# Optimization experiments

Hardware: AMD Instinct MI355X
Metric: run time of the kernel (lower is better)

The kernel has to match this reference:

```python
import jax, jax.numpy as jnp
import numpy as np

EPS_COS = 1e-8   # torch cosine_similarity eps
ATT_EPS = 1e-6   # LinearAttention eps
LN_EPS = 1e-5    # nn.LayerNorm default eps
NHEAD = 8
WS = 8           # window_size
TOPK = 16
C = 256          # embed_dim (hardcoded 256 in original gather)


def layer_norm(x, w, b):
    m = x.mean(-1, keepdims=True)
    v = ((x - m) ** 2).mean(-1, keepdims=True)
    return (x - m) / jnp.sqrt(v + LN_EPS) * w + b


def linear_attention(q, k, v):
    # q,k,v: [N, L, H, D]
    Q = jax.nn.elu(q) + 1.0
    K = jax.nn.elu(k) + 1.0
    L = v.shape[1]
    v = v / L
    KV = jnp.einsum('nshd,nshv->nhdv', K, v)
    Z = 1.0 / (jnp.einsum('nlhd,nhd->nlh', Q, K.sum(axis=1)) + ATT_EPS)
    return jnp.einsum('nlhd,nhdv,nlh->nlhv', Q, KV, Z) * L


def encoder_layer(x, source, Wq, Wk, Wv, Wm, W1, W2, n1w, n1b, n2w, n2b):
    bs, _, d = x.shape
    dim = d // NHEAD
    q = (x @ Wq).reshape(bs, -1, NHEAD, dim)
    k = (source @ Wk).reshape(bs, -1, NHEAD, dim)
    v = (source @ Wv).reshape(bs, -1, NHEAD, dim)
    msg = linear_attention(q, k, v).reshape(bs, -1, d) @ Wm
    msg = layer_norm(msg, n1w, n1b)
    msg = jax.nn.relu(jnp.concatenate([x, msg], axis=-1) @ W1) @ W2
    msg = layer_norm(msg, n2w, n2b)
    return x + msg


def topk_select(x, k):
    # x: [BN, S, C]; cosine similarity of each token to window mean, then topk
    avg = x.mean(axis=1, keepdims=True)                        # [BN,1,C]
    dot = (avg * x).sum(axis=-1)                               # [BN,S]
    na = jnp.maximum(jnp.linalg.norm(avg, axis=-1), EPS_COS)   # [BN,1]
    nb = jnp.maximum(jnp.linalg.norm(x, axis=-1), EPS_COS)     # [BN,S]
    cos = dot / (na * nb)
    _, idx = jax.lax.top_k(cos, k)                             # [BN,k]
    sel = jnp.take_along_axis(x, idx[:, :, None], axis=1)      # [BN,k,C]
    return sel, idx


def scatter_add(x, idx, src):
    # x: [BN,S,C], idx: [BN,k], src: [BN,k,C]
    BN, S, c = x.shape
    flat_idx = (jnp.arange(BN)[:, None] * S + idx).reshape(-1)
    return x.reshape(BN * S, c).at[flat_idx].add(src.reshape(-1, c)).reshape(BN, S, c)


def window_reverse_nchw(windows, ws, H, W):
    c = windows.shape[-1]
    x = windows.transpose(0, 2, 1).reshape(-1, H // ws, W // ws, c, ws, ws)
    return x.transpose(0, 3, 1, 4, 2, 5).reshape(-1, c, H, W)


def setup_inputs() -> dict:
    key = jax.random.key(0)
    ks = jax.random.split(key, 8)
    BN = 2 * 2304  # batch * nums_window
    s = 1.0 / np.sqrt(C)
    return {
        'x_win_attn': jax.random.normal(ks[0], (BN, WS * WS, C), jnp.float32),
        's_win_attn': jax.random.normal(ks[1], (BN, WS * WS, C), jnp.float32),
        'Wq': jax.random.normal(ks[2], (C, C), jnp.float32) * s,
        'Wk': jax.random.normal(ks[3], (C, C), jnp.float32) * s,
        'Wv': jax.random.normal(ks[4], (C, C), jnp.float32) * s,
        'Wmerge': jax.random.normal(ks[5], (C, C), jnp.float32) * s,
        'W1': jax.random.normal(ks[6], (2 * C, 2 * C), jnp.float32) * (1.0 / np.sqrt(2 * C)),
        'W2': jax.random.normal(ks[7], (2 * C, C), jnp.float32) * (1.0 / np.sqrt(2 * C)),
        'n1w': jnp.ones((C,), jnp.float32),
        'n1b': jnp.zeros((C,), jnp.float32),
        'n2w': jnp.ones((C,), jnp.float32),
        'n2b': jnp.zeros((C,), jnp.float32),
        'batch_size': 2,
        'nums_window': 2304,
        'h': 384,
        'w': 384,
    }


def reference(x_win_attn, s_win_attn, Wq, Wk, Wv, Wmerge, W1, W2,
              n1w, n1b, n2w, n2b, batch_size, nums_window, h, w):
    # 'cross' attention path of WinTopKAttention
    sel1, idx1 = topk_select(x_win_attn, TOPK)
    sel2, _ = topk_select(s_win_attn, TOPK)
    sel1 = sel1.reshape(batch_size, nums_window * TOPK, C)
    sel2 = sel2.reshape(batch_size, nums_window * TOPK, C)
    out = encoder_layer(sel1, sel2, Wq, Wk, Wv, Wmerge, W1, W2, n1w, n1b, n2w, n2b)
    out = out.reshape(batch_size * nums_window, TOPK, C)
    combined = scatter_add(x_win_attn, idx1, out)
    return window_reverse_nchw(combined, WS, h, w)
```

## Files before the change

### kernel.cpp

```cpp
#include <hip/hip_runtime.h>
#include <math.h>

static constexpr int BATCH = 2;
static constexpr int NWIN  = 2304;
static constexpr int BN    = BATCH * NWIN;
static constexpr int S     = 64;
static constexpr int CDIM  = 256;
static constexpr int TOPK_ = 16;
static constexpr int TROWS = BN * TOPK_;
static constexpr int LB    = NWIN * TOPK_;
static constexpr int HW    = 384;
static constexpr int KVSZ  = 8448;
static constexpr int KVB   = 384;
static constexpr int KVTOK = LB / KVB;

typedef unsigned short u16;
typedef __attribute__((ext_vector_type(4))) float  f32x4;
typedef __attribute__((ext_vector_type(8))) short  bf16x8;

__device__ inline u16 f2bf(float f) {
    unsigned u = __float_as_uint(f);
    return (u16)((u + 0x7fffu + ((u >> 16) & 1u)) >> 16);
}
__device__ inline float bf2f(u16 b) {
    return __uint_as_float(((unsigned)b) << 16);
}

__device__ inline void load_lds16(const void* g, void* l) {
    __builtin_amdgcn_global_load_lds(
        (const __attribute__((address_space(1))) unsigned int*)g,
        (__attribute__((address_space(3))) unsigned int*)l, 16, 0, 0);
}

__global__ __launch_bounds__(256) void wconv_all_k(
    const float* __restrict__ Wq, const float* __restrict__ Wk,
    const float* __restrict__ Wv, const float* __restrict__ Wm,
    const float* __restrict__ W1, const float* __restrict__ W2,
    u16* __restrict__ Wqt, u16* __restrict__ Wkt, u16* __restrict__ Wvt,
    u16* __restrict__ Wmt, u16* __restrict__ W1t, u16* __restrict__ W2t)
{
    int t = blockIdx.x * 256 + threadIdx.x;
    const float* W; u16* Wt; int Nd, Kd;
    if (t < 262144) {
        const int sel = t >> 16; t &= 65535;
        W  = (sel == 0 ? Wq  : sel == 1 ? Wk  : sel == 2 ? Wv  : Wm);
        Wt = (sel == 0 ? Wqt : sel == 1 ? Wkt : sel == 2 ? Wvt : Wmt);
        Nd = 256; Kd = 256;
    } else if (t < 524288) { W = W1; Wt = W1t; Nd = 512; Kd = 512; t -= 262144; }
    else                   { W = W2; Wt = W2t; Nd = 256; Kd = 512; t -= 524288; }
    const int k = t / Nd, n = t - k * Nd;
    Wt[(size_t)n * Kd + k] = f2bf(W[t]);
}

__global__ __launch_bounds__(512) void topk_gather_k(
    const float* __restrict__ xin, const float* __restrict__ sin,
    u16* __restrict__ catp, u16* __restrict__ selS, int* __restrict__ idxX)
{
    __shared__ float  win[64 * 256];
    __shared__ double red[2][256];
    __shared__ double avgd[256];
    __shared__ double cosv[64];
    __shared__ int    slots[16];

    const int w    = blockIdx.x;
    const bool isX = (blockIdx.y == 0);
    const int tid  = threadIdx.x;
    const float* src = (isX ? xin : sin) + (size_t)w * S * CDIM;

#pragma unroll
    for (int k = 0; k < 8; ++k) {
        load_lds16(src + k * 2048 + tid * 4,
                   &win[k * 2048 + (tid >> 6) * 256]);
    }
    __syncthreads();

    {
        const int h = tid >> 8, c = tid & 255;
        double sm = 0.0;
        for (int t = h * 32; t < h * 32 + 32; ++t)
            sm += (double)win[t * 256 + c];
        red[h][c] = sm;
    }
    __syncthreads();
    if (tid < 256) avgd[tid] = (red[0][tid] + red[1][tid]) * (1.0 / 64.0);
    __syncthreads();

    {
        const int tok = tid >> 3, p = tid & 7;
        double sd = 0.0, sn = 0.0;
#pragma unroll
        for (int i = 0; i < 8; ++i) {
            const int ic = (i + tok) & 7;
            const int c0 = p * 32 + ic * 4;
            const f32x4 xv4 = *(const f32x4*)&win[tok * 256 + c0];
#pragma unroll
            for (int q = 0; q < 4; ++q) {
                const double xv = (double)xv4[q];
                sd += avgd[c0 + q] * xv;
                sn += xv * xv;
            }
        }
        sd += __shfl_xor(sd, 1); sd += __shfl_xor(sd, 2); sd += __shfl_xor(sd, 4);
        sn += __shfl_xor(sn, 1); sn += __shfl_xor(sn, 2); sn += __shfl_xor(sn, 4);
        if (p == 0) {
            double nb = sqrt(sn); if (nb < 1e-8) nb = 1e-8;
            cosv[tok] = sd / nb;
        }
    }
    __syncthreads();

    if (tid < 64) {
        const double ct = cosv[tid];
        int r = 0;
        for (int j = 0; j < 64; ++j) {
            const double cj = cosv[j];
            r += (cj > ct) || (cj == ct && j < tid);
        }
        if (r < TOPK_) slots[r] = tid;
    }
    __syncthreads();

    const int c = tid & 255, g = tid >> 8;
    if (isX) {
        if (tid < TOPK_) idxX[w * TOPK_ + tid] = slots[tid];
#pragma unroll
        for (int jj = 0; jj < 8; ++jj) {
            const int j = g * 8 + jj;
            catp[((size_t)w * TOPK_ + j) * 512 + c] = f2bf(win[slots[j] * 256 + c]);
        }
    } else {
#pragma unroll
        for (int jj = 0; jj < 8; ++jj) {
            const int j = g * 8 + jj;
            selS[((size_t)w * TOPK_ + j) * 256 + c] = f2bf(win[slots[j] * 256 + c]);
        }
    }
}

template<int EPI>
__device__ inline void gemm_body(
    const u16* __restrict__ A, int lda,
    const u16* __restrict__ Bt, int K,
    u16* __restrict__ Cout, int ldc,
    int m0, int n0, u16* As, u16* Bs)
{
    const int tid = threadIdx.x;
    const int lane = tid & 63, w = tid >> 6;
    const int wr = w >> 1, wc = w & 1;

    f32x4 acc[4][4];
#pragma unroll
    for (int i = 0; i < 4; ++i)
#pragma unroll
        for (int j = 0; j < 4; ++j)
            acc[i][j] = (f32x4){0.f, 0.f, 0.f, 0.f};

    const int rsel = lane & 15, ksel = (lane >> 4) * 8;

    for (int k0 = 0; k0 < K; k0 += 32) {
#pragma unroll
        for (int i = 0; i < 2; ++i) {
            const int c = w * 2 + i;
            const int e = c * 512 + lane * 8;
            const int row = e >> 5, col = e & 31;
            load_lds16(&A[(size_t)(m0 + row) * lda + k0 + col], &As[c * 512]);
            load_lds16(&Bt[(size_t)(n0 + row) * K  + k0 + col], &Bs[c * 512]);
        }
        __syncthreads();

        bf16x8 af[4], bfr[4];
#pragma unroll
        for (int i = 0; i < 4; ++i)
            af[i] = *(const bf16x8*)&As[(wr * 64 + i * 16 + rsel) * 32 + ksel];
#pragma unroll
        for (int j = 0; j < 4; ++j)
            bfr[j] = *(const bf16x8*)&Bs[(wc * 64 + j * 16 + rsel) * 32 + ksel];
#pragma unroll
        for (int i = 0; i < 4; ++i)
#pragma unroll
            for (int j = 0; j < 4; ++j)
                acc[i][j] = __builtin_amdgcn_mfma_f32_16x16x32_bf16(
                    af[i], bfr[j], acc[i][j], 0, 0, 0);
        __syncthreads();
    }

    const int crow = (lane >> 4) * 4, ccol = lane & 15;
#pragma unroll
    for (int i = 0; i < 4; ++i)
#pragma unroll
        for (int j = 0; j < 4; ++j)
#pragma unroll
            for (int r = 0; r < 4; ++r) {
                float v = acc[i][j][r];
                if (EPI == 1) v = (v > 0.f) ? (v + 1.f) : __expf(v);
                if (EPI == 2) v = (v > 0.f) ? v : 0.f;
                Cout[(size_t)(m0 + wr * 64 + i * 16 + crow + r) * ldc
                     + (n0 + wc * 64 + j * 16 + ccol)] = f2bf(v);
            }
}

template<int EPI>
__global__ __launch_bounds__(256) void gemm_bf16_k(
    const u16* __restrict__ A, int lda,
    const u16* __restrict__ Bt, int K,
    u16* __restrict__ Cout, int ldc)
{
    __shared__ u16 As[128 * 32];
    __shared__ u16 Bs[128 * 32];
    gemm_body<EPI>(A, lda, Bt, K, Cout, ldc,
                   blockIdx.y * 128, blockIdx.x * 128, As, Bs);
}

__global__ __launch_bounds__(256) void gemm_qkv_k(
    const u16* __restrict__ catA, const u16* __restrict__ selS,
    const u16* __restrict__ Wqt, const u16* __restrict__ Wkt,
    const u16* __restrict__ Wvt,
    u16* __restrict__ Qb, u16* __restrict__ Kb, u16* __restrict__ Vb)
{
    __shared__ u16 As[128 * 32];
    __shared__ u16 Bs[128 * 32];
    const int z = blockIdx.z;
    if (z == 0)
        gemm_body<1>(catA, 512, Wqt, 256, Qb, 256,
                     blockIdx.y * 128, blockIdx.x * 128, As, Bs);
    else if (z == 1)
        gemm_body<1>(selS, 256, Wkt, 256, Kb, 256,
                     blockIdx.y * 128, blockIdx.x * 128, As, Bs);
    else
        gemm_body<0>(selS, 256, Wvt, 256, Vb, 256,
                     blockIdx.y * 128, blockIdx.x * 128, As, Bs);
}

__global__ __launch_bounds__(256) void kv_part_k(
    const u16* __restrict__ Kb, const u16* __restrict__ Vb,
    float* __restrict__ part)
{
    __shared__ float Kt[16][256];
    __shared__ float Vt[16][256];

    const int bk = blockIdx.x;
    const int batch = bk / KVB, slot = bk % KVB;
    const size_t r0 = (size_t)batch * LB + (size_t)slot * KVTOK;
    const int h = threadIdx.x >> 5, e = threadIdx.x & 31;

    float acc[32] = {};
    float ks = 0.f;

    for (int tile = 0; tile < KVTOK / 16; ++tile) {
        const size_t rb = r0 + tile * 16;
        for (int i = 0; i < 16; ++i) {
            Kt[i][threadIdx.x] = bf2f(Kb[(rb + i) * 256 + threadIdx.x]);
            Vt[i][threadIdx.x] = bf2f(Vb[(rb + i) * 256 + threadIdx.x]);
        }
        __syncthreads();
        for (int s = 0; s < 16; ++s) {
            const float vv = Vt[s][(h << 5) + e];
            ks += Kt[s][(h << 5) + e];
#pragma unroll
            for (int d = 0; d < 32; ++d)
                acc[d] += Kt[s][(h << 5) + d] * vv;
        }
        __syncthreads();
    }

    float* pb = part + (size_t)bk * KVSZ;
    for (int d = 0; d < 32; ++d)
        pb[((h << 5) + d) * 32 + e] = acc[d];
    pb[8192 + threadIdx.x] = ks;
}

__global__ __launch_bounds__(256) void kv_reduce_k(
    const float* __restrict__ part, float* __restrict__ fin)
{
    __shared__ float r2[4][64];
    const int chunk = blockIdx.x;
    const int b = chunk / (KVSZ / 64);
    const int i0 = (chunk % (KVSZ / 64)) * 64;
    const int il = threadIdx.x & 63, pg = threadIdx.x >> 6;

    float s = 0.f;
    for (int p = pg; p < KVB; p += 4)
        s += part[(size_t)(b * KVB + p) * KVSZ + i0 + il];
    r2[pg][il] = s;
    __syncthreads();
    if (threadIdx.x < 64)
        fin[(size_t)b * KVSZ + i0 + threadIdx.x] =
            r2[0][threadIdx.x] + r2[1][threadIdx.x] +
            r2[2][threadIdx.x] + r2[3][threadIdx.x];
}

__global__ __launch_bounds__(256) void attn_apply_k(
    const u16* __restrict__ Q, const float* __restrict__ KV,
    u16* __restrict__ outp)
{
    __shared__ float kvs[8192];
    __shared__ float kss[256];
    __shared__ float qs[8][256];

    const int t0 = blockIdx.x * 64;
    const int batch = t0 / LB;
    const float* kvb = KV + (size_t)batch * KVSZ;
    for (int i = threadIdx.x; i < 8192; i += 256) kvs[i] = kvb[i];
    kss[threadIdx.x] = kvb[8192 + threadIdx.x];
    const int h = threadIdx.x >> 5, e = threadIdx.x & 31;
    __syncthreads();

    for (int o = 0; o < 64; o += 8) {
        __syncthreads();
        for (int i = 0; i < 8; ++i)
            qs[i][threadIdx.x] = bf2f(Q[(size_t)(t0 + o + i) * 256 + threadIdx.x]);
        __syncthreads();
        for (int tt = 0; tt < 8; ++tt) {
            const float* qh = &qs[tt][h << 5];
            float zq = 0.f, res = 0.f;
#pragma unroll
            for (int d = 0; d < 32; ++d) {
                const float qd = qh[d];
                zq  += qd * kss[(h << 5) + d];
                res += qd * kvs[((h << 5) + d) * 32 + e];
            }
            outp[(size_t)(t0 + o + tt) * 256 + threadIdx.x] = f2bf(res / (zq + 1e-6f));
        }
    }
}

template<bool ADDG>
__global__ __launch_bounds__(256) void ln_k(
    const u16* __restrict__ in, u16* __restrict__ outp, int ldo,
    const float* __restrict__ gw, const float* __restrict__ gb,
    const float* __restrict__ xsrc, const int* __restrict__ idx)
{
    const int lane = threadIdx.x & 63, wid = threadIdx.x >> 6;
    const size_t row = (size_t)blockIdx.x * 4 + wid;
    const u16* ip = in + row * 256;

    float xv[4];
#pragma unroll
    for (int i = 0; i < 4; ++i) xv[i] = bf2f(ip[i * 64 + lane]);
    float s = xv[0] + xv[1] + xv[2] + xv[3];
#pragma unroll
    for (int m = 1; m < 64; m <<= 1) s += __shfl_xor(s, m);
    const float mean = s * (1.f / 256.f);
    float v = 0.f;
#pragma unroll
    for (int i = 0; i < 4; ++i) { const float d = xv[i] - mean; v += d * d; }
#pragma unroll
    for (int m = 1; m < 64; m <<= 1) v += __shfl_xor(v, m);
    const float rstd = rsqrtf(v * (1.f / 256.f) + 1e-5f);

    const float* xr = nullptr;
    if (ADDG) xr = xsrc + ((size_t)(row >> 4) * 64 + idx[row]) * 256;

#pragma unroll
    for (int i = 0; i < 4; ++i) {
        const int c = i * 64 + lane;
        float o = (xv[i] - mean) * rstd * gw[c] + gb[c];
        if (ADDG) o += xr[c];
        outp[row * ldo + c] = f2bf(o);
    }
}

__global__ __launch_bounds__(256) void combine_reverse_k(
    const float* __restrict__ xin, const int* __restrict__ idxX,
    const u16* __restrict__ outsel, float* __restrict__ outp)
{
    __shared__ float tile[128 * 33];
    __shared__ int   sidx[32];

    const int p  = blockIdx.x;
    const int c0 = blockIdx.y * 32;
    const int b  = p / 1152;
    const int rem = p % 1152;
    const int wy  = rem / 24, wxp = rem % 24;
    const int w0  = b * NWIN + wy * 48 + wxp * 2;
    const int tid = threadIdx.x;

    if (tid < 32) sidx[tid] = idxX[(w0 + (tid >> 4)) * TOPK_ + (tid & 15)];

    {
        const int r = tid >> 1, half = tid & 1;
        const int wl = r >> 6, t = r & 63;
        const float* srcp = xin + ((size_t)(w0 + wl) * 64 + t) * 256 + c0 + half * 16;
        const float4 v0 = ((const float4*)srcp)[0];
        const float4 v1 = ((const float4*)srcp)[1];
        const float4 v2 = ((const float4*)srcp)[2];
        const float4 v3 = ((const float4*)srcp)[3];
        float* dst = &tile[r * 33 + half * 16];
        dst[0] = v0.x; dst[1] = v0.y; dst[2]  = v0.z; dst[3]  = v0.w;
        dst[4] = v1.x; dst[5] = v1.y; dst[6]  = v1.z; dst[7]  = v1.w;
        dst[8] = v2.x; dst[9] = v2.y; dst[10] = v2.z; dst[11] = v2.w;
        dst[12] = v3.x; dst[13] = v3.y; dst[14] = v3.z; dst[15] = v3.w;
    }
    __syncthreads();

    for (int it = 0; it < 4; ++it) {
        const int rid = it * 8 + (tid >> 5);
        const int cc  = tid & 31;
        const int wl  = rid >> 4, j = rid & 15;
        const int t   = sidx[rid];
        tile[((wl << 6) + t) * 33 + cc] +=
            bf2f(outsel[((size_t)(w0 + wl) * TOPK_ + j) * 256 + c0 + cc]);
    }
    __syncthreads();

    const int chalf = tid >> 7;
    const int pix = tid & 127;
    const int dy = pix >> 4, x16 = pix & 15;
    const int wl = x16 >> 3, dx = x16 & 7;
    const int rr = (wl << 6) + dy * 8 + dx;
    const size_t obase = (((size_t)b * 256 + c0 + chalf) * HW + (wy * 8 + dy)) * HW
                       + wxp * 16 + x16;
    for (int cc = 0; cc < 32; cc += 2)
        outp[obase + (size_t)cc * (HW * HW)] = tile[rr * 33 + cc + chalf];
}

extern "C" void kernel_launch(void* const* d_in, const int* in_sizes, int n_in,
                              void* d_out, int out_size, void* d_ws, size_t ws_size,
                              hipStream_t stream)
{
    const float* x   = (const float*)d_in[0];
    const float* s   = (const float*)d_in[1];
    const float* Wq  = (const float*)d_in[2];
    const float* Wk  = (const float*)d_in[3];
    const float* Wv  = (const float*)d_in[4];
    const float* Wm  = (const float*)d_in[5];
    const float* W1  = (const float*)d_in[6];
    const float* W2  = (const float*)d_in[7];
    const float* n1w = (const float*)d_in[8];
    const float* n1b = (const float*)d_in[9];
    const float* n2w = (const float*)d_in[10];
    const float* n2b = (const float*)d_in[11];
    float* out = (float*)d_out;

    char* ws = (char*)d_ws;
    int*   idxX   = (int*)ws;
    float* KVpart = (float*)(ws + 294912);
    float* KVfin  = (float*)(ws + 26247168);
    u16*   Wqt    = (u16*)(ws + 26314752);
    u16*   Wkt    = (u16*)(ws + 26445824);
    u16*   Wvt    = (u16*)(ws + 26576896);
    u16*   Wmt    = (u16*)(ws + 26707968);
    u16*   W1t    = (u16*)(ws + 26839040);
    u16*   W2t    = (u16*)(ws + 27363328);
    u16*   Qb     = (u16*)(ws + 27625472);
    u16*   Kb     = (u16*)(ws + 65374208);
    u16*   Vb     = (u16*)(ws + 103122944);
    u16*   Mb     = (u16*)(ws + 140871680);
    u16*   osel   = (u16*)(ws + 178620416);

    u16* catA  = (u16*)d_out;
    u16* selSb = (u16*)((char*)d_out + 75497472);
    u16* msgA  = (u16*)((char*)d_out + 113246208);
    u16* Hb    = (u16*)((char*)d_out + 150994944);

    wconv_all_k<<<dim3(2560), 256, 0, stream>>>(Wq, Wk, Wv, Wm, W1, W2,
                                                Wqt, Wkt, Wvt, Wmt, W1t, W2t);

    topk_gather_k<<<dim3(BN, 2), 512, 0, stream>>>(x, s, catA, selSb, idxX);

    gemm_qkv_k<<<dim3(2, 576, 3), 256, 0, stream>>>(catA, selSb, Wqt, Wkt, Wvt,
                                                    Qb, Kb, Vb);

    kv_part_k<<<dim3(2 * KVB), 256, 0, stream>>>(Kb, Vb, KVpart);
    kv_reduce_k<<<dim3(2 * (KVSZ / 64)), 256, 0, stream>>>(KVpart, KVfin);

    attn_apply_k<<<dim3(TROWS / 64), 256, 0, stream>>>(Qb, KVfin, msgA);

    gemm_bf16_k<0><<<dim3(2, 576), 256, 0, stream>>>(msgA, 256, Wmt, 256, Mb, 256);
    ln_k<false><<<dim3(TROWS / 4), 256, 0, stream>>>(Mb, catA + 256, 512, n1w, n1b, nullptr, nullptr);

    gemm_bf16_k<2><<<dim3(4, 576), 256, 0, stream>>>(catA, 512, W1t, 512, Hb, 512);
    gemm_bf16_k<0><<<dim3(2, 576), 256, 0, stream>>>(Hb, 512, W2t, 512, Mb, 256);

    ln_k<true><<<dim3(TROWS / 4), 256, 0, stream>>>(Mb, osel, 256, n2w, n2b, x, idxX);

    combine_reverse_k<<<dim3(BN / 2, 8), 256, 0, stream>>>(x, idxX, osel, out);
}
```

Before: 716.9 us.

## Keep window tile in registers for topk selection instead of LDS staging

The top-k gather kernel now loads each window's 64x256 fp32 tile directly into registers, not into a 64 KB LDS buffer. Column sums, per-thread partial dot products and norms are computed from those registers. Only small double partials go to LDS, and the selected rows are written out as packed 64-bit bf16 stores. This cuts LDS footprint, which should raise occupancy, and removes the LDS reread for the gather. In exchange, register pressure rises and the partial reduction order changes slightly.

```diff
diff --git a/kernel.cpp b/kernel.cpp
--- a/kernel.cpp
+++ b/kernel.cpp
@@ -15,6 +15,7 @@
 static constexpr int KVTOK = LB / KVB;
 
 typedef unsigned short u16;
+typedef unsigned long long u64;
 typedef __attribute__((ext_vector_type(4))) float  f32x4;
 typedef __attribute__((ext_vector_type(8))) short  bf16x8;
 
@@ -56,49 +57,66 @@
     const float* __restrict__ xin, const float* __restrict__ sin,
     u16* __restrict__ catp, u16* __restrict__ selS, int* __restrict__ idxX)
 {
-    __shared__ float  win[64 * 256];
-    __shared__ double red[2][256];
-    __shared__ double avgd[256];
-    __shared__ double cosv[64];
-    __shared__ int    slots[16];
+    __shared__ double2 pd[64 * 65];
+    __shared__ double  avgd[256];
+    __shared__ double  cosv[64];
+    __shared__ int     rk[64];
+    __shared__ int     slots[16];
 
     const int w    = blockIdx.x;
     const bool isX = (blockIdx.y == 0);
     const int tid  = threadIdx.x;
+    const int cg   = tid & 63, rg = tid >> 6;
     const float* src = (isX ? xin : sin) + (size_t)w * S * CDIM;
 
-#pragma unroll
-    for (int k = 0; k < 8; ++k) {
-        load_lds16(src + k * 2048 + tid * 4,
-                   &win[k * 2048 + (tid >> 6) * 256]);
+    f32x4 v[8];
+#pragma unroll
+    for (int m = 0; m < 8; ++m)
+        v[m] = *(const f32x4*)&src[(rg + 8 * m) * CDIM + cg * 4];
+
+    double cs[4] = {0.0, 0.0, 0.0, 0.0};
+#pragma unroll
+    for (int m = 0; m < 8; ++m)
+#pragma unroll
+        for (int q = 0; q < 4; ++q)
+            cs[q] += (double)v[m][q];
+
+    double* red = (double*)pd;
+#pragma unroll
+    for (int q = 0; q < 4; ++q)
+        red[rg * 256 + cg * 4 + q] = cs[q];
+    __syncthreads();
+
+    if (tid < 256) {
+        double sm = 0.0;
+#pragma unroll
+        for (int r = 0; r < 8; ++r) sm += red[r * 256 + tid];
+        avgd[tid] = sm * (1.0 / 64.0);
     }
     __syncthreads();
 
     {
-        const int h = tid >> 8, c = tid & 255;
-        double sm = 0.0;
-        for (int t = h * 32; t < h * 32 + 32; ++t)
-            sm += (double)win[t * 256 + c];
-        red[h][c] = sm;
-    }
-    __syncthreads();
-    if (tid < 256) avgd[tid] = (red[0][tid] + red[1][tid]) * (1.0 / 64.0);
+        const double a0 = avgd[cg * 4 + 0], a1 = avgd[cg * 4 + 1];
+        const double a2 = avgd[cg * 4 + 2], a3 = avgd[cg * 4 + 3];
+        __syncthreads();
+#pragma unroll
+        for (int m = 0; m < 8; ++m) {
+            const double x0 = (double)v[m][0], x1 = (double)v[m][1];
+            const double x2 = (double)v[m][2], x3 = (double)v[m][3];
+            double d = a0 * x0; d += a1 * x1; d += a2 * x2; d += a3 * x3;
+            double n = x0 * x0; n += x1 * x1; n += x2 * x2; n += x3 * x3;
+            pd[(rg + 8 * m) * 65 + cg] = (double2){d, n};
+        }
+    }
     __syncthreads();
 
     {
         const int tok = tid >> 3, p = tid & 7;
         double sd = 0.0, sn = 0.0;
 #pragma unroll
-        for (int i = 0; i < 8; ++i) {
-            const int ic = (i + tok) & 7;
-            const int c0 = p * 32 + ic * 4;
-            const f32x4 xv4 = *(const f32x4*)&win[tok * 256 + c0];
-#pragma unroll
-            for (int q = 0; q < 4; ++q) {
-                const double xv = (double)xv4[q];
-                sd += avgd[c0 + q] * xv;
-                sn += xv * xv;
-            }
+        for (int j = 0; j < 8; ++j) {
+            const double2 t2 = pd[tok * 65 + p * 8 + j];
+            sd += t2.x; sn += t2.y;
         }
         sd += __shfl_xor(sd, 1); sd += __shfl_xor(sd, 2); sd += __shfl_xor(sd, 4);
         sn += __shfl_xor(sn, 1); sn += __shfl_xor(sn, 2); sn += __shfl_xor(sn, 4);
@@ -116,23 +134,21 @@
             const double cj = cosv[j];
             r += (cj > ct) || (cj == ct && j < tid);
         }
+        rk[tid] = r;
         if (r < TOPK_) slots[r] = tid;
     }
     __syncthreads();
 
-    const int c = tid & 255, g = tid >> 8;
-    if (isX) {
-        if (tid < TOPK_) idxX[w * TOPK_ + tid] = slots[tid];
-#pragma unroll
-        for (int jj = 0; jj < 8; ++jj) {
-            const int j = g * 8 + jj;
-            catp[((size_t)w * TOPK_ + j) * 512 + c] = f2bf(win[slots[j] * 256 + c]);
-        }
-    } else {
-#pragma unroll
-        for (int jj = 0; jj < 8; ++jj) {
-            const int j = g * 8 + jj;
-            selS[((size_t)w * TOPK_ + j) * 256 + c] = f2bf(win[slots[j] * 256 + c]);
+    if (isX && tid < TOPK_) idxX[w * TOPK_ + tid] = slots[tid];
+#pragma unroll
+    for (int m = 0; m < 8; ++m) {
+        const int r = rg + 8 * m;
+        const int j = rk[r];
+        if (j < TOPK_) {
+            u64 pk = (u64)f2bf(v[m][0]) | ((u64)f2bf(v[m][1]) << 16)
+                   | ((u64)f2bf(v[m][2]) << 32) | ((u64)f2bf(v[m][3]) << 48);
+            if (isX) *(u64*)&catp[((size_t)w * TOPK_ + j) * 512 + cg * 4] = pk;
+            else     *(u64*)&selS[((size_t)w * TOPK_ + j) * 256 + cg * 4] = pk;
         }
     }
 }
```

After: 712.4 us. No clear change (-0.6%).
